# Kernel optimization log

Measured on AMD Instinct MI355X. Metric: run time of the kernel, lower is better.

## Reference

```python
import jax, jax.numpy as jnp
import numpy as np

N_NODES = 100000
N_EDGES = 3200000


def gcn_conv(x, W, b, src, dst, n_nodes):
    # x: [N, Fin] -> [N, Fout]; PyG GCNConv: linear, add self-loops,
    # symmetric norm D^-1/2 A_hat D^-1/2, sum-aggregate over incoming edges, + bias
    h = x @ W  # [N, Fout]
    loop = jnp.arange(n_nodes, dtype=src.dtype)
    src2 = jnp.concatenate([src, loop])
    dst2 = jnp.concatenate([dst, loop])
    deg = jax.ops.segment_sum(jnp.ones_like(dst2, dtype=h.dtype), dst2, num_segments=n_nodes)
    dinv = jnp.where(deg > 0, jax.lax.rsqrt(deg), 0.0)
    norm = dinv[src2] * dinv[dst2]  # [E+N]
    msgs = h[src2] * norm[:, None]  # gather + scale
    out = jax.ops.segment_sum(msgs, dst2, num_segments=n_nodes)  # scatter-add
    return out + b


def setup_inputs() -> dict:
    key = jax.random.key(0)
    k1, k2, k3, k4 = jax.random.split(key, 4)
    x = jax.random.normal(k1, (N_NODES, 16), dtype=jnp.float32)
    edge_index = jax.random.randint(k2, (2, N_EDGES), 0, N_NODES, dtype=jnp.int64)
    W1 = jax.random.normal(k3, (16, 32), dtype=jnp.float32) * (1.0 / np.sqrt(16))
    b1 = jnp.zeros((32,), dtype=jnp.float32)
    W2 = jax.random.normal(k4, (32, 3), dtype=jnp.float32) * (1.0 / np.sqrt(32))
    b2 = jnp.zeros((3,), dtype=jnp.float32)
    return {"x": x, "edge_index": edge_index, "W1": W1, "b1": b1, "W2": W2, "b2": b2}


def reference(x, edge_index, W1, b1, W2, b2):
    src, dst = edge_index[0], edge_index[1]
    n = x.shape[0]
    h = gcn_conv(x, W1, b1, src, dst, n)
    h = jax.nn.relu(h)
    h = gcn_conv(h, W2, b2, src, dst, n)
    return jax.nn.log_softmax(h, axis=1)
```

## Files before the change

kernel.cpp:

```cpp
#include <hip/hip_runtime.h>
#include <math.h>


#define NN 100000
#define NE 3200000
#define BSH 7
#define NPB 128
#define NB  ((NN + NPB - 1) / NPB)
#define EPB 12544
#define CAP 6144
#define SCAP 5120

__device__ __forceinline__ float bl(unsigned u) { return __uint_as_float(u << 16); }
__device__ __forceinline__ float bh(unsigned u) { return __uint_as_float(u & 0xFFFF0000u); }
__device__ __forceinline__ unsigned rne(float f) {
    unsigned u = __float_as_uint(f);
    return (u + 0x7FFFu + ((u >> 16) & 1u)) >> 16;
}

typedef int vint4 __attribute__((ext_vector_type(4)));


__global__ void __launch_bounds__(256) k_zero(int* __restrict__ bcur) {
    int t = blockIdx.x * 256 + threadIdx.x;
    if (t < NB) bcur[t] = 0;
}

__global__ void __launch_bounds__(512) k_partition(
        const int* __restrict__ src, const int* __restrict__ dst,
        int* __restrict__ bcur, unsigned int* __restrict__ ebuf, int E) {
    __shared__ int hist[NB];
    __shared__ int lbase[NB];
    __shared__ int gbase[NB];
    __shared__ int lcur[NB];
    __shared__ unsigned int sebuf[EPB];
    __shared__ unsigned short sbkt[EPB];
    __shared__ int wsum[8];
    __shared__ int t1_s;
    int tid = threadIdx.x;
    int e0 = blockIdx.x * EPB;
    int e1 = min(e0 + EPB, E);
    int cnt = e1 - e0;
    int cnt4 = cnt >> 2;
    for (int t = tid; t < NB; t += 512) { hist[t] = 0; lcur[t] = 0; }
    __syncthreads();
    const vint4* d4 = (const vint4*)(dst + e0);
    vint4 dc[7];
#pragma unroll
    for (int r = 0; r < 7; r++) {
        int i4 = r * 512 + tid;
        if (i4 < cnt4) {
            dc[r] = d4[i4];
            atomicAdd(&hist[dc[r].x >> BSH], 1);
            atomicAdd(&hist[dc[r].y >> BSH], 1);
            atomicAdd(&hist[dc[r].z >> BSH], 1);
            atomicAdd(&hist[dc[r].w >> BSH], 1);
        }
    }
    __syncthreads();
    int lane = tid & 63, w = tid >> 6;
    {
        int v = hist[tid];
        int incl = v;
#pragma unroll
        for (int off = 1; off < 64; off <<= 1) {
            int u = __shfl_up(incl, off);
            if (lane >= off) incl += u;
        }
        if (lane == 63) wsum[w] = incl;
        __syncthreads();
        int woff = 0, tot = 0;
#pragma unroll
        for (int k = 0; k < 8; k++) { tot += wsum[k]; woff += (k < w) ? wsum[k] : 0; }
        int excl = incl - v + woff;
        lbase[tid] = excl;
        gbase[tid] = tid * CAP + (v ? atomicAdd(&bcur[tid], v) : 0);
        if (tid == 0) t1_s = tot;
        __syncthreads();
    }
    {
        int b2 = 512 + tid;
        int v = (b2 < NB) ? hist[b2] : 0;
        int incl = v;
#pragma unroll
        for (int off = 1; off < 64; off <<= 1) {
            int u = __shfl_up(incl, off);
            if (lane >= off) incl += u;
        }
        if (lane == 63) wsum[w] = incl;
        __syncthreads();
        int woff = 0;
#pragma unroll
        for (int k = 0; k < 8; k++) woff += (k < w) ? wsum[k] : 0;
        int excl = incl - v + woff + t1_s;
        if (b2 < NB) {
            lbase[b2] = excl;
            gbase[b2] = b2 * CAP + (v ? atomicAdd(&bcur[b2], v) : 0);
        }
        __syncthreads();
    }
    const vint4* s4 = (const vint4*)(src + e0);
#pragma unroll
    for (int r = 0; r < 7; r++) {
        int i4 = r * 512 + tid;
        if (i4 < cnt4) {
            vint4 sv = s4[i4];
            int d, b, p;
            d = dc[r].x; b = d >> BSH; p = lbase[b] + atomicAdd(&lcur[b], 1);
            sebuf[p] = (unsigned)sv.x | ((unsigned)(d & (NPB - 1)) << 20);
            sbkt[p] = (unsigned short)b;
            d = dc[r].y; b = d >> BSH; p = lbase[b] + atomicAdd(&lcur[b], 1);
            sebuf[p] = (unsigned)sv.y | ((unsigned)(d & (NPB - 1)) << 20);
            sbkt[p] = (unsigned short)b;
            d = dc[r].z; b = d >> BSH; p = lbase[b] + atomicAdd(&lcur[b], 1);
            sebuf[p] = (unsigned)sv.z | ((unsigned)(d & (NPB - 1)) << 20);
            sbkt[p] = (unsigned short)b;
            d = dc[r].w; b = d >> BSH; p = lbase[b] + atomicAdd(&lcur[b], 1);
            sebuf[p] = (unsigned)sv.w | ((unsigned)(d & (NPB - 1)) << 20);
            sbkt[p] = (unsigned short)b;
        }
    }
    __syncthreads();
    for (int p = tid; p < cnt; p += 512) {
        int b = sbkt[p];
        ebuf[gbase[b] + (p - lbase[b])] = sebuf[p];
    }
}

__global__ void __launch_bounds__(256) k_csr(
        const unsigned int* __restrict__ ebuf, const int* __restrict__ bcur,
        const float* __restrict__ x, int* __restrict__ col,
        unsigned int* __restrict__ rowinfo, float* __restrict__ dinv,
        unsigned int* __restrict__ xsb, int N) {
    __shared__ unsigned int se[SCAP];
    __shared__ int hist[NPB];
    __shared__ int base[NPB];
    __shared__ int lcur[NPB];
    __shared__ int wsum[4];
    int b = blockIdx.x;
    int tid = threadIdx.x;
    int beg = b * CAP;
    int cnt = bcur[b];
    int cl = min(cnt, SCAP);
    if (tid < NPB) { hist[tid] = 0; lcur[tid] = 0; }
    __syncthreads();
    for (int j = tid; j < cl; j += 256) {
        unsigned pe = __builtin_nontemporal_load(&ebuf[beg + j]);
        se[j] = pe;
        atomicAdd(&hist[pe >> 20], 1);
    }
    for (int j = SCAP + tid; j < cnt; j += 256)
        atomicAdd(&hist[ebuf[beg + j] >> 20], 1);
    __syncthreads();
    int lane = tid & 63, w = tid >> 6;
    int v = (tid < NPB) ? hist[tid] : 0;
    int incl = v;
#pragma unroll
    for (int off = 1; off < 64; off <<= 1) {
        int u = __shfl_up(incl, off);
        if (lane >= off) incl += u;
    }
    if (lane == 63) wsum[w] = incl;
    __syncthreads();
    int woff = 0;
#pragma unroll
    for (int k = 0; k < 4; k++) woff += (k < w) ? wsum[k] : 0;
    int excl = incl - v + woff;
    int node = b * NPB + tid;
    if (tid < NPB) {
        base[tid] = excl;
        if (node < N) {
            float di = rsqrtf((float)(v + 1));
            dinv[node] = di;
            rowinfo[node] = ((unsigned)(beg + excl) << 8) | (unsigned)v;
            const float4* x4 = (const float4*)(x + (size_t)node * 16);
            float4 A = x4[0], B = x4[1], C = x4[2], D = x4[3];
            uint4 o0, o1;
            o0.x = rne(A.x * di) | (rne(A.y * di) << 16);
            o0.y = rne(A.z * di) | (rne(A.w * di) << 16);
            o0.z = rne(B.x * di) | (rne(B.y * di) << 16);
            o0.w = rne(B.z * di) | (rne(B.w * di) << 16);
            o1.x = rne(C.x * di) | (rne(C.y * di) << 16);
            o1.y = rne(C.z * di) | (rne(C.w * di) << 16);
            o1.z = rne(D.x * di) | (rne(D.y * di) << 16);
            o1.w = rne(D.z * di) | (rne(D.w * di) << 16);
            uint4* op = (uint4*)xsb;
            op[(size_t)node * 2 + 0] = o0;
            op[(size_t)node * 2 + 1] = o1;
        }
    }
    __syncthreads();
    for (int j = tid; j < cl; j += 256) {
        unsigned pe = se[j];
        int dl = pe >> 20;
        int pos = beg + base[dl] + atomicAdd(&lcur[dl], 1);
        col[pos] = (int)(pe & 0xFFFFF);
    }
    for (int j = SCAP + tid; j < cnt; j += 256) {
        unsigned pe = ebuf[beg + j];
        int dl = pe >> 20;
        int pos = beg + base[dl] + atomicAdd(&lcur[dl], 1);
        col[pos] = (int)(pe & 0xFFFFF);
    }
}

__global__ void __launch_bounds__(256) k_agg(
        const unsigned int* __restrict__ rowinfo, const int* __restrict__ col,
        const unsigned int* __restrict__ xsb, unsigned int* __restrict__ aggb,
        int N) {
    int wv = (int)((blockIdx.x * 256 + threadIdx.x) >> 6);
    int lane = threadIdx.x & 63;
    int q = lane >> 4;
    int wid = wv * 4 + q;
    if (wid >= N) return;
    int lq = lane & 15;
    int r = lq >> 2, c = lq & 3;
    unsigned info = rowinfo[wid];
    int beg = (int)(info >> 8);
    int end = beg + (int)(info & 255u);
    const uint2* xb = (const uint2*)xsb;
    float a0 = 0.f, a1 = 0.f, a2 = 0.f, a3 = 0.f;
    int j = beg + r;
    while (j + 12 < end) {
        int s0 = col[j], s1 = col[j + 4], s2 = col[j + 8], s3 = col[j + 12];
        uint2 q0 = xb[(size_t)s0 * 4 + c];
        uint2 q1 = xb[(size_t)s1 * 4 + c];
        uint2 q2 = xb[(size_t)s2 * 4 + c];
        uint2 q3 = xb[(size_t)s3 * 4 + c];
        a0 += bl(q0.x); a1 += bh(q0.x); a2 += bl(q0.y); a3 += bh(q0.y);
        a0 += bl(q1.x); a1 += bh(q1.x); a2 += bl(q1.y); a3 += bh(q1.y);
        a0 += bl(q2.x); a1 += bh(q2.x); a2 += bl(q2.y); a3 += bh(q2.y);
        a0 += bl(q3.x); a1 += bh(q3.x); a2 += bl(q3.y); a3 += bh(q3.y);
        j += 16;
    }
    while (j < end) {
        int s = col[j];
        uint2 qq = xb[(size_t)s * 4 + c];
        a0 += bl(qq.x); a1 += bh(qq.x); a2 += bl(qq.y); a3 += bh(qq.y);
        j += 4;
    }
#pragma unroll
    for (int off = 8; off >= 4; off >>= 1) {
        a0 += __shfl_down(a0, off);
        a1 += __shfl_down(a1, off);
        a2 += __shfl_down(a2, off);
        a3 += __shfl_down(a3, off);
    }
    if (lq < 4) {
        uint2 qq = xb[(size_t)wid * 4 + lq];
        a0 += bl(qq.x); a1 += bh(qq.x); a2 += bl(qq.y); a3 += bh(qq.y);
        uint2 o;
        o.x = rne(a0) | (rne(a1) << 16);
        o.y = rne(a2) | (rne(a3) << 16);
        ((uint2*)aggb)[(size_t)wid * 4 + lq] = o;
    }
}

__global__ void __launch_bounds__(256) k_h(
        const unsigned int* __restrict__ aggb, const float* __restrict__ dinv,
        const float* __restrict__ W1, const float* __restrict__ b1,
        const float* __restrict__ W2, unsigned int* __restrict__ g2b, int N) {
    __shared__ float W1s[16 * 32];
    __shared__ float W2s[96];
    __shared__ float b1s[32];
    for (int t = threadIdx.x; t < 512; t += 256) W1s[t] = W1[t];
    if (threadIdx.x < 96) W2s[threadIdx.x] = W2[threadIdx.x];
    if (threadIdx.x < 32) b1s[threadIdx.x] = b1[threadIdx.x];
    __syncthreads();
    int i = blockIdx.x * 256 + threadIdx.x;
    if (i >= N) return;
    const uint4* ab = (const uint4*)aggb;
    uint4 q0 = ab[(size_t)i * 2 + 0];
    uint4 q1 = ab[(size_t)i * 2 + 1];
    float a[16] = {bl(q0.x), bh(q0.x), bl(q0.y), bh(q0.y),
                   bl(q0.z), bh(q0.z), bl(q0.w), bh(q0.w),
                   bl(q1.x), bh(q1.x), bl(q1.y), bh(q1.y),
                   bl(q1.z), bh(q1.z), bl(q1.w), bh(q1.w)};
    float di = dinv[i];
    float p0 = 0.f, p1 = 0.f, p2 = 0.f;
#pragma unroll
    for (int jj = 0; jj < 32; jj++) {
        float o = 0.f;
#pragma unroll
        for (int k = 0; k < 16; k++) o = fmaf(a[k], W1s[k * 32 + jj], o);
        float z = fmaxf(fmaf(di, o, b1s[jj]), 0.f);
        p0 = fmaf(z, W2s[jj * 3 + 0], p0);
        p1 = fmaf(z, W2s[jj * 3 + 1], p1);
        p2 = fmaf(z, W2s[jj * 3 + 2], p2);
    }
    uint2 o;
    o.x = rne(p0 * di) | (rne(p1 * di) << 16);
    o.y = rne(p2 * di);
    ((uint2*)g2b)[i] = o;
}

__global__ void __launch_bounds__(256) k_l2(
        const unsigned int* __restrict__ rowinfo, const int* __restrict__ col,
        const unsigned int* __restrict__ g2b, const float* __restrict__ dinv,
        const float* __restrict__ b2, float* __restrict__ out, int N) {
    int wid = (int)((blockIdx.x * 256 + threadIdx.x) >> 3);
    if (wid >= N) return;
    int lo = threadIdx.x & 7;
    unsigned info = rowinfo[wid];
    int beg = (int)(info >> 8);
    int end = beg + (int)(info & 255u);
    const uint2* gb = (const uint2*)g2b;
    float a0 = 0.f, a1 = 0.f, a2 = 0.f;
    int j = beg + lo;
    while (j + 8 < end) {
        uint2 v0 = gb[col[j]];
        uint2 v1 = gb[col[j + 8]];
        a0 += bl(v0.x); a1 += bh(v0.x); a2 += bl(v0.y);
        a0 += bl(v1.x); a1 += bh(v1.x); a2 += bl(v1.y);
        j += 16;
    }
    if (j < end) {
        uint2 v = gb[col[j]];
        a0 += bl(v.x); a1 += bh(v.x); a2 += bl(v.y);
    }
#pragma unroll
    for (int off = 4; off >= 1; off >>= 1) {
        a0 += __shfl_down(a0, off);
        a1 += __shfl_down(a1, off);
        a2 += __shfl_down(a2, off);
    }
    if (lo == 0) {
        float di = dinv[wid];
        uint2 sv = gb[wid];
        float v0 = fmaf(di, a0 + bl(sv.x), b2[0]);
        float v1 = fmaf(di, a1 + bh(sv.x), b2[1]);
        float v2 = fmaf(di, a2 + bl(sv.y), b2[2]);
        float m = fmaxf(v0, fmaxf(v1, v2));
        float lse = m + logf(expf(v0 - m) + expf(v1 - m) + expf(v2 - m));
        out[(size_t)wid * 3 + 0] = v0 - lse;
        out[(size_t)wid * 3 + 1] = v1 - lse;
        out[(size_t)wid * 3 + 2] = v2 - lse;
    }
}


extern "C" void kernel_launch(void* const* d_in, const int* in_sizes, int n_in,
                              void* d_out, int out_size, void* d_ws, size_t ws_size,
                              hipStream_t stream) {
    const float* x  = (const float*)d_in[0];
    const int*   ei = (const int*)d_in[1];
    const float* W1 = (const float*)d_in[2];
    const float* b1 = (const float*)d_in[3];
    const float* W2 = (const float*)d_in[4];
    const float* b2 = (const float*)d_in[5];
    float* out = (float*)d_out;

    const int* src = ei;
    const int* dst = ei + NE;

    unsigned int* ebuf = (unsigned int*)d_ws;
    int*          col  = (int*)(ebuf + (size_t)NB * CAP);
    unsigned int* xsb  = (unsigned int*)(col + (size_t)NB * CAP);
    unsigned int* aggb = xsb + (size_t)NN * 8;
    unsigned int* g2b  = aggb + (size_t)NN * 8;
    float*        dinv = (float*)(g2b + (size_t)NN * 2);
    unsigned int* rowinfo = (unsigned int*)(dinv + NN);
    int*          bcur = (int*)(rowinfo + NN);

    const int B = 256;
    int gbP = (NE + EPB - 1) / EPB;
    int gbS = (NN + B - 1) / B;
    int gbW1 = (NN * 16 + B - 1) / B;
    int gbW2 = (NN * 8 + B - 1) / B;
    int gbZ = (NB + B - 1) / B;

    k_zero<<<gbZ, B, 0, stream>>>(bcur);
    k_partition<<<gbP, 512, 0, stream>>>(src, dst, bcur, ebuf, NE);
    k_csr<<<NB, B, 0, stream>>>(ebuf, bcur, x, col, rowinfo, dinv, xsb, NN);
    k_agg<<<gbW1, B, 0, stream>>>(rowinfo, col, xsb, aggb, NN);
    k_h<<<gbS, B, 0, stream>>>(aggb, dinv, W1, b1, W2, g2b, NN);
    k_l2<<<gbW2, B, 0, stream>>>(rowinfo, col, g2b, dinv, b2, out, NN);
}
```

Baseline: 96.60 us.

## Fuse layer-1 aggregation with dense transform into one kernel

Merges the first-layer neighbor aggregation kernel with the per-node W1/ReLU/W2 transform kernel. Aggregated 16-feature rows now stay in shared memory instead of being rounded to bf16 and round-tripped through a global buffer. The matmul is spread across 16 lanes per node and finished with shuffle reductions. This saves one launch and the intermediate global traffic, but adds a block-wide barrier after the irregular gather and loads the weights into shared memory in every block (gbW1 blocks of 16 nodes each rather than 256).

```diff
diff --git a/kernel.cpp b/kernel.cpp
--- a/kernel.cpp
+++ b/kernel.cpp
@@ -204,94 +204,96 @@
     }
 }
 
-__global__ void __launch_bounds__(256) k_agg(
+__global__ void __launch_bounds__(256) k_aggh(
         const unsigned int* __restrict__ rowinfo, const int* __restrict__ col,
-        const unsigned int* __restrict__ xsb, unsigned int* __restrict__ aggb,
-        int N) {
-    int wv = (int)((blockIdx.x * 256 + threadIdx.x) >> 6);
-    int lane = threadIdx.x & 63;
+        const unsigned int* __restrict__ xsb, const float* __restrict__ dinv,
+        const float* __restrict__ W1, const float* __restrict__ b1,
+        const float* __restrict__ W2, unsigned int* __restrict__ g2b, int N) {
+    __shared__ float sacc[16][16];
+    __shared__ float W1s[512];
+    __shared__ float W2s[96];
+    __shared__ float b1s[32];
+    int tid = threadIdx.x;
+    for (int t = tid; t < 512; t += 256) W1s[t] = W1[t];
+    if (tid < 96) W2s[tid] = W2[tid];
+    if (tid < 32) b1s[tid] = b1[tid];
+    int lane = tid & 63;
     int q = lane >> 4;
-    int wid = wv * 4 + q;
-    if (wid >= N) return;
+    int nib = (tid >> 6) * 4 + q;
+    int wid = blockIdx.x * 16 + nib;
     int lq = lane & 15;
     int r = lq >> 2, c = lq & 3;
-    unsigned info = rowinfo[wid];
-    int beg = (int)(info >> 8);
-    int end = beg + (int)(info & 255u);
     const uint2* xb = (const uint2*)xsb;
-    float a0 = 0.f, a1 = 0.f, a2 = 0.f, a3 = 0.f;
-    int j = beg + r;
-    while (j + 12 < end) {
-        int s0 = col[j], s1 = col[j + 4], s2 = col[j + 8], s3 = col[j + 12];
-        uint2 q0 = xb[(size_t)s0 * 4 + c];
-        uint2 q1 = xb[(size_t)s1 * 4 + c];
-        uint2 q2 = xb[(size_t)s2 * 4 + c];
-        uint2 q3 = xb[(size_t)s3 * 4 + c];
-        a0 += bl(q0.x); a1 += bh(q0.x); a2 += bl(q0.y); a3 += bh(q0.y);
-        a0 += bl(q1.x); a1 += bh(q1.x); a2 += bl(q1.y); a3 += bh(q1.y);
-        a0 += bl(q2.x); a1 += bh(q2.x); a2 += bl(q2.y); a3 += bh(q2.y);
-        a0 += bl(q3.x); a1 += bh(q3.x); a2 += bl(q3.y); a3 += bh(q3.y);
-        j += 16;
-    }
-    while (j < end) {
-        int s = col[j];
-        uint2 qq = xb[(size_t)s * 4 + c];
-        a0 += bl(qq.x); a1 += bh(qq.x); a2 += bl(qq.y); a3 += bh(qq.y);
-        j += 4;
-    }
-#pragma unroll
-    for (int off = 8; off >= 4; off >>= 1) {
-        a0 += __shfl_down(a0, off);
-        a1 += __shfl_down(a1, off);
-        a2 += __shfl_down(a2, off);
-        a3 += __shfl_down(a3, off);
-    }
-    if (lq < 4) {
-        uint2 qq = xb[(size_t)wid * 4 + lq];
-        a0 += bl(qq.x); a1 += bh(qq.x); a2 += bl(qq.y); a3 += bh(qq.y);
+    if (wid < N) {
+        unsigned info = rowinfo[wid];
+        int beg = (int)(info >> 8);
+        int end = beg + (int)(info & 255u);
+        float a0 = 0.f, a1 = 0.f, a2 = 0.f, a3 = 0.f;
+        int j = beg + r;
+        while (j + 12 < end) {
+            int s0 = col[j], s1 = col[j + 4], s2 = col[j + 8], s3 = col[j + 12];
+            uint2 q0 = xb[(size_t)s0 * 4 + c];
+            uint2 q1 = xb[(size_t)s1 * 4 + c];
+            uint2 q2 = xb[(size_t)s2 * 4 + c];
+            uint2 q3 = xb[(size_t)s3 * 4 + c];
+            a0 += bl(q0.x); a1 += bh(q0.x); a2 += bl(q0.y); a3 += bh(q0.y);
+            a0 += bl(q1.x); a1 += bh(q1.x); a2 += bl(q1.y); a3 += bh(q1.y);
+            a0 += bl(q2.x); a1 += bh(q2.x); a2 += bl(q2.y); a3 += bh(q2.y);
+            a0 += bl(q3.x); a1 += bh(q3.x); a2 += bl(q3.y); a3 += bh(q3.y);
+            j += 16;
+        }
+        while (j < end) {
+            int s = col[j];
+            uint2 qq = xb[(size_t)s * 4 + c];
+            a0 += bl(qq.x); a1 += bh(qq.x); a2 += bl(qq.y); a3 += bh(qq.y);
+            j += 4;
+        }
+#pragma unroll
+        for (int off = 8; off >= 4; off >>= 1) {
+            a0 += __shfl_down(a0, off);
+            a1 += __shfl_down(a1, off);
+            a2 += __shfl_down(a2, off);
+            a3 += __shfl_down(a3, off);
+        }
+        if (lq < 4) {
+            uint2 qq = xb[(size_t)wid * 4 + lq];
+            sacc[nib][lq * 4 + 0] = a0 + bl(qq.x);
+            sacc[nib][lq * 4 + 1] = a1 + bh(qq.x);
+            sacc[nib][lq * 4 + 2] = a2 + bl(qq.y);
+            sacc[nib][lq * 4 + 3] = a3 + bh(qq.y);
+        }
+    }
+    __syncthreads();
+    int nib2 = tid >> 4, j16 = tid & 15;
+    int node = blockIdx.x * 16 + nib2;
+    float p0 = 0.f, p1 = 0.f, p2 = 0.f, di = 0.f;
+    if (node < N) {
+        di = dinv[node];
+        float h0 = 0.f, h1 = 0.f;
+#pragma unroll
+        for (int k = 0; k < 16; k++) {
+            float ak = sacc[nib2][k];
+            h0 = fmaf(ak, W1s[k * 32 + j16], h0);
+            h1 = fmaf(ak, W1s[k * 32 + j16 + 16], h1);
+        }
+        float z0 = fmaxf(fmaf(di, h0, b1s[j16]), 0.f);
+        float z1 = fmaxf(fmaf(di, h1, b1s[j16 + 16]), 0.f);
+        p0 = fmaf(z1, W2s[(j16 + 16) * 3 + 0], z0 * W2s[j16 * 3 + 0]);
+        p1 = fmaf(z1, W2s[(j16 + 16) * 3 + 1], z0 * W2s[j16 * 3 + 1]);
+        p2 = fmaf(z1, W2s[(j16 + 16) * 3 + 2], z0 * W2s[j16 * 3 + 2]);
+    }
+#pragma unroll
+    for (int off = 8; off >= 1; off >>= 1) {
+        p0 += __shfl_down(p0, off);
+        p1 += __shfl_down(p1, off);
+        p2 += __shfl_down(p2, off);
+    }
+    if (j16 == 0 && node < N) {
         uint2 o;
-        o.x = rne(a0) | (rne(a1) << 16);
-        o.y = rne(a2) | (rne(a3) << 16);
-        ((uint2*)aggb)[(size_t)wid * 4 + lq] = o;
-    }
-}
-
-__global__ void __launch_bounds__(256) k_h(
-        const unsigned int* __restrict__ aggb, const float* __restrict__ dinv,
-        const float* __restrict__ W1, const float* __restrict__ b1,
-        const float* __restrict__ W2, unsigned int* __restrict__ g2b, int N) {
-    __shared__ float W1s[16 * 32];
-    __shared__ float W2s[96];
-    __shared__ float b1s[32];
-    for (int t = threadIdx.x; t < 512; t += 256) W1s[t] = W1[t];
-    if (threadIdx.x < 96) W2s[threadIdx.x] = W2[threadIdx.x];
-    if (threadIdx.x < 32) b1s[threadIdx.x] = b1[threadIdx.x];
-    __syncthreads();
-    int i = blockIdx.x * 256 + threadIdx.x;
-    if (i >= N) return;
-    const uint4* ab = (const uint4*)aggb;
-    uint4 q0 = ab[(size_t)i * 2 + 0];
-    uint4 q1 = ab[(size_t)i * 2 + 1];
-    float a[16] = {bl(q0.x), bh(q0.x), bl(q0.y), bh(q0.y),
-                   bl(q0.z), bh(q0.z), bl(q0.w), bh(q0.w),
-                   bl(q1.x), bh(q1.x), bl(q1.y), bh(q1.y),
-                   bl(q1.z), bh(q1.z), bl(q1.w), bh(q1.w)};
-    float di = dinv[i];
-    float p0 = 0.f, p1 = 0.f, p2 = 0.f;
-#pragma unroll
-    for (int jj = 0; jj < 32; jj++) {
-        float o = 0.f;
-#pragma unroll
-        for (int k = 0; k < 16; k++) o = fmaf(a[k], W1s[k * 32 + jj], o);
-        float z = fmaxf(fmaf(di, o, b1s[jj]), 0.f);
-        p0 = fmaf(z, W2s[jj * 3 + 0], p0);
-        p1 = fmaf(z, W2s[jj * 3 + 1], p1);
-        p2 = fmaf(z, W2s[jj * 3 + 2], p2);
-    }
-    uint2 o;
-    o.x = rne(p0 * di) | (rne(p1 * di) << 16);
-    o.y = rne(p2 * di);
-    ((uint2*)g2b)[i] = o;
+        o.x = rne(p0 * di) | (rne(p1 * di) << 16);
+        o.y = rne(p2 * di);
+        ((uint2*)g2b)[node] = o;
+    }
 }
 
 __global__ void __launch_bounds__(256) k_l2(
@@ -356,15 +358,13 @@
     unsigned int* ebuf = (unsigned int*)d_ws;
     int*          col  = (int*)(ebuf + (size_t)NB * CAP);
     unsigned int* xsb  = (unsigned int*)(col + (size_t)NB * CAP);
-    unsigned int* aggb = xsb + (size_t)NN * 8;
-    unsigned int* g2b  = aggb + (size_t)NN * 8;
+    unsigned int* g2b  = xsb + (size_t)NN * 8;
     float*        dinv = (float*)(g2b + (size_t)NN * 2);
     unsigned int* rowinfo = (unsigned int*)(dinv + NN);
     int*          bcur = (int*)(rowinfo + NN);
 
     const int B = 256;
     int gbP = (NE + EPB - 1) / EPB;
-    int gbS = (NN + B - 1) / B;
     int gbW1 = (NN * 16 + B - 1) / B;
     int gbW2 = (NN * 8 + B - 1) / B;
     int gbZ = (NB + B - 1) / B;
@@ -372,7 +372,6 @@
     k_zero<<<gbZ, B, 0, stream>>>(bcur);
     k_partition<<<gbP, 512, 0, stream>>>(src, dst, bcur, ebuf, NE);
     k_csr<<<NB, B, 0, stream>>>(ebuf, bcur, x, col, rowinfo, dinv, xsb, NN);
-    k_agg<<<gbW1, B, 0, stream>>>(rowinfo, col, xsb, aggb, NN);
-    k_h<<<gbS, B, 0, stream>>>(aggb, dinv, W1, b1, W2, g2b, NN);
+    k_aggh<<<gbW1, B, 0, stream>>>(rowinfo, col, xsb, dinv, W1, b1, W2, g2b, NN);
     k_l2<<<gbW2, B, 0, stream>>>(rowinfo, col, g2b, dinv, b2, out, NN);
 }
```

Measured after the change: 98.70 us. 2.2% more time.
